# Performance work log

Measured on AMD Instinct MI355X. Metric: run time of the kernel, lower is better.

## Reference

```python
import jax, jax.numpy as jnp
import numpy as np

C_CT, C_MRI, C_OUT = 64, 64, 64
B, D, H, W = 1, 8, 32, 32


def setup_inputs() -> dict:
    key = jax.random.key(0)
    ks = jax.random.split(key, 18)
    s = 0.05
    inp = {
        "ct_features": jax.random.normal(ks[0], (B, C_CT, D, H, W), jnp.float32),
        "mri_features": jax.random.normal(ks[1], (B, C_MRI, D, H, W), jnp.float32),
        # 1x1x1 Conv3d == per-voxel linear: weight (out, in), bias (out,)
        "wq_ct": jax.random.normal(ks[2], (C_OUT, C_CT), jnp.float32) * s,
        "bq_ct": jax.random.normal(ks[3], (C_OUT,), jnp.float32) * s,
        "wk_mri": jax.random.normal(ks[4], (C_OUT, C_MRI), jnp.float32) * s,
        "bk_mri": jax.random.normal(ks[5], (C_OUT,), jnp.float32) * s,
        "wv_mri": jax.random.normal(ks[6], (C_OUT, C_MRI), jnp.float32) * s,
        "bv_mri": jax.random.normal(ks[7], (C_OUT,), jnp.float32) * s,
        "wq_mri": jax.random.normal(ks[8], (C_OUT, C_MRI), jnp.float32) * s,
        "bq_mri": jax.random.normal(ks[9], (C_OUT,), jnp.float32) * s,
        "wk_ct": jax.random.normal(ks[10], (C_OUT, C_CT), jnp.float32) * s,
        "bk_ct": jax.random.normal(ks[11], (C_OUT,), jnp.float32) * s,
        "wv_ct": jax.random.normal(ks[12], (C_OUT, C_CT), jnp.float32) * s,
        "bv_ct": jax.random.normal(ks[13], (C_OUT,), jnp.float32) * s,
        "wo": jax.random.normal(ks[14], (C_OUT, 2 * C_OUT), jnp.float32) * s,
        "bo": jax.random.normal(ks[15], (C_OUT,), jnp.float32) * s,
    }
    return inp


def _proj(x_flat, w, b):
    # x_flat: (B, Cin, N); 1x1x1 conv -> (B, Cout, N)
    return jnp.einsum("oc,bcn->bon", w, x_flat) + b[None, :, None]


def _forward(ct, mri, wq_ct, bq_ct, wk_mri, bk_mri, wv_mri, bv_mri,
             wq_mri, bq_mri, wk_ct, bk_ct, wv_ct, bv_ct, wo, bo):
    b, _, d, h, w = ct.shape
    n = d * h * w
    ct_f = ct.reshape(b, ct.shape[1], n)
    mri_f = mri.reshape(b, mri.shape[1], n)
    scale = 1.0 / np.sqrt(C_OUT).astype(np.float32)

    # CT queries attend over MRI keys/values
    ct_q = _proj(ct_f, wq_ct, bq_ct)      # (B, C, N)
    mri_k = _proj(mri_f, wk_mri, bk_mri)  # (B, C, N)
    mri_v = _proj(mri_f, wv_mri, bv_mri)  # (B, C, N)
    attn_ct = jax.nn.softmax(jnp.einsum("bci,bcj->bij", ct_q, mri_k) * scale, axis=-1)
    ct_att = jnp.einsum("bcj,bij->bci", mri_v, attn_ct)  # (B, C, N)

    # MRI queries attend over CT keys/values
    mri_q = _proj(mri_f, wq_mri, bq_mri)
    ct_k = _proj(ct_f, wk_ct, bk_ct)
    ct_v = _proj(ct_f, wv_ct, bv_ct)
    attn_mri = jax.nn.softmax(jnp.einsum("bci,bcj->bij", mri_q, ct_k) * scale, axis=-1)
    mri_att = jnp.einsum("bcj,bij->bci", ct_v, attn_mri)

    fused = jnp.concatenate([ct_att, mri_att], axis=1)  # (B, 2C, N)
    out = _proj(fused, wo, bo)  # (B, C, N)
    return out.reshape(b, C_OUT, d, h, w)


def reference(ct_features, mri_features, wq_ct, bq_ct, wk_mri, bk_mri,
              wv_mri, bv_mri, wq_mri, bq_mri, wk_ct, bk_ct, wv_ct, bv_ct,
              wo, bo):
    return _forward(ct_features, mri_features, wq_ct, bq_ct, wk_mri, bk_mri,
                    wv_mri, bv_mri, wq_mri, bq_mri, wk_ct, bk_ct,
                    wv_ct, bv_ct, wo, bo)
```

## Files before the change

### kernel.cpp

```cpp
#include <hip/hip_runtime.h>
#include <stdint.h>

constexpr int N = 8192;
constexpr float QSCALE = 0.18033688011112042f;
constexpr int SPLIT = 4;

typedef __attribute__((ext_vector_type(4))) float f32x4;
typedef __attribute__((ext_vector_type(4))) unsigned int u32x4;
typedef __attribute__((ext_vector_type(2))) unsigned int u32x2;
typedef __attribute__((ext_vector_type(4))) unsigned short u16x4;

__device__ inline unsigned short f2bf(float f) {
  unsigned u = __builtin_bit_cast(unsigned, f);
  u += 0x7FFFu + ((u >> 16) & 1u);
  return (unsigned short)(u >> 16);
}
__device__ inline float bf2f(unsigned short u) {
  return __builtin_bit_cast(float, (unsigned)u << 16);
}
__device__ inline unsigned cvtpk(float a, float b) {
  unsigned r;
  asm("v_cvt_pk_bf16_f32 %0, %1, %2" : "=v"(r) : "v"(a), "v"(b));
  return r;
}

__device__ inline void mfma16x16x32bf16(f32x4& d, u32x4 a, u32x4 b) {
  asm volatile("v_mfma_f32_16x16x32_bf16 %0, %1, %2, %0" : "+v"(d) : "v"(a), "v"(b));
}
__device__ inline void mfma_guard() {
  __builtin_amdgcn_sched_barrier(0);
  asm volatile("s_nop 7\n\ts_nop 7");
  __builtin_amdgcn_sched_barrier(0);
}
__device__ inline void gload16(const void* src, void* lds) {
  __builtin_amdgcn_global_load_lds(
      (const __attribute__((address_space(1))) unsigned int*)src,
      (__attribute__((address_space(3))) unsigned int*)lds, 16, 0, 0);
}

struct ProjArgs {
  const float* x[6];
  const float* w[6];
  const float* b[6];
  unsigned short* o[6];
  int mode[6];
  float scale[6];
};

__global__ __launch_bounds__(256) void proj_kernel(ProjArgs A) {
  const int p = blockIdx.y;
  const float* __restrict__ x = A.x[p];
  const float* __restrict__ w = A.w[p];
  const float* __restrict__ bias = A.b[p];
  unsigned short* __restrict__ out = A.o[p];
  const int n0 = blockIdx.x * 64;
  __shared__ float Xs[64][64];
  __shared__ float Ws[64][64];
  const int t = threadIdx.x;
#pragma unroll
  for (int i = 0; i < 4; i++) {
    int s = t + i * 256;
    ((u32x4*)Ws)[s] = ((const u32x4*)w)[s];
  }
#pragma unroll
  for (int i = 0; i < 4; i++) {
    int s = t + i * 256;
    int c = s >> 4, nc = s & 15;
    *(u32x4*)&Xs[c][nc * 4] = *(const u32x4*)&x[c * N + n0 + nc * 4];
  }
  __syncthreads();
  const int n = t & 63, h = t >> 6;
  float acc[16];
#pragma unroll
  for (int o = 0; o < 16; o++) acc[o] = bias[h * 16 + o];
  for (int c = 0; c < 64; c++) {
    float xv = Xs[c][n];
#pragma unroll
    for (int o = 0; o < 16; o++) acc[o] = fmaf(Ws[h * 16 + o][c], xv, acc[o]);
  }
  const float sc = A.scale[p];
  if (A.mode[p] == 0) {
    unsigned short* po = out + (size_t)(n0 + n) * 64 + h * 16;
#pragma unroll
    for (int o = 0; o < 16; o++) po[o] = f2bf(acc[o] * sc);
  } else {
#pragma unroll
    for (int o = 0; o < 16; o++) out[(size_t)(h * 16 + o) * N + n0 + n] = f2bf(acc[o] * sc);
  }
}

__global__ __launch_bounds__(256, 2) void attn_kernel(
    const unsigned short* __restrict__ Q0, const unsigned short* __restrict__ K0,
    const unsigned short* __restrict__ V0, const unsigned short* __restrict__ Q1,
    const unsigned short* __restrict__ K1, const unsigned short* __restrict__ V1,
    unsigned short* __restrict__ Opart, float* __restrict__ Lsum) {
  const int bid = blockIdx.x;
  const int slice = bid & 7;
  const int qb = bid >> 3;
  const int dir = slice >> 2;
  const int chunk = slice & 3;
  const unsigned short* __restrict__ Q = dir ? Q1 : Q0;
  const unsigned short* __restrict__ K = dir ? K1 : K0;
  const unsigned short* __restrict__ V = dir ? V1 : V0;

  __shared__ char smem[65536];

  const int t = threadIdx.x;
  const int lane = t & 63, w = t >> 6;
  const int g = lane >> 4, sl = lane & 15;
  char* const pw = smem + 49152 + w * 4096;
  const int kvbase = chunk * 2048;

  const int srowoff = (lane >> 3);
  const int swzb = ((lane & 7) ^ (lane >> 3)) * 16;
  const char* const Kc = (const char*)K;
  const char* const Vc = (const char*)V;

  u32x4 qf[2][2];
#pragma unroll
  for (int rb = 0; rb < 2; rb++) {
    const int qrow = qb * 128 + w * 32 + rb * 16 + sl;
#pragma unroll
    for (int ks = 0; ks < 2; ks++)
      qf[rb][ks] = *(const u32x4*)(Q + (size_t)qrow * 64 + ks * 32 + 8 * g);
  }

  f32x4 acc[4][2];
#pragma unroll
  for (int mb = 0; mb < 4; mb++)
#pragma unroll
    for (int rb = 0; rb < 2; rb++)
#pragma unroll
      for (int r = 0; r < 4; r++) acc[mb][rb][r] = 0.f;
  float lpart[2] = {0.f, 0.f};

#pragma unroll
  for (int tt = 0; tt < 2; tt++) {
    const int j0 = kvbase + tt * 64;
#pragma unroll
    for (int i = 0; i < 2; i++) {
      const int row = (w * 2 + i) * 8 + srowoff;
      gload16(Kc + (size_t)(j0 + row) * 128 + swzb,
              smem + tt * 8192 + (w * 2 + i) * 1024);
      gload16(Vc + (size_t)row * (N * 2) + (size_t)j0 * 2 + swzb,
              smem + 24576 + tt * 8192 + (w * 2 + i) * 1024);
    }
  }

  int cur = 0;
  for (int jt = 0; jt < 32; ++jt) {
    if (jt < 31) asm volatile("s_waitcnt vmcnt(4)" ::: "memory");
    else         asm volatile("s_waitcnt vmcnt(0)" ::: "memory");
    __builtin_amdgcn_s_barrier();
    __builtin_amdgcn_sched_barrier(0);

    if (jt + 2 < 32) {
      const int j0n = kvbase + (jt + 2) * 64;
      const int nb = (cur >= 1) ? cur - 1 : 2;
#pragma unroll
      for (int i = 0; i < 2; i++) {
        const int row = (w * 2 + i) * 8 + srowoff;
        gload16(Kc + (size_t)(j0n + row) * 128 + swzb,
                smem + nb * 8192 + (w * 2 + i) * 1024);
        gload16(Vc + (size_t)row * (N * 2) + (size_t)j0n * 2 + swzb,
                smem + 24576 + nb * 8192 + (w * 2 + i) * 1024);
      }
    }
    char* const Kl = smem + cur * 8192;
    char* const Vl = smem + 24576 + cur * 8192;

    u32x4 kf[4][2];
#pragma unroll
    for (int jb = 0; jb < 4; jb++) {
      const int row = jb * 16 + sl;
      const int rs = (row & 7) << 4;
#pragma unroll
      for (int ks = 0; ks < 2; ks++)
        kf[jb][ks] = *(const u32x4*)(Kl + row * 128 + ((ks * 64 + 16 * g) ^ rs));
    }

    f32x4 st[4][2];
    __builtin_amdgcn_s_setprio(1);
#pragma unroll
    for (int jb = 0; jb < 4; jb++)
#pragma unroll
      for (int rb = 0; rb < 2; rb++) {
#pragma unroll
        for (int r = 0; r < 4; r++) st[jb][rb][r] = 0.f;
        mfma16x16x32bf16(st[jb][rb], kf[jb][0], qf[rb][0]);
        mfma16x16x32bf16(st[jb][rb], kf[jb][1], qf[rb][1]);
      }
    __builtin_amdgcn_s_setprio(0);
    mfma_guard();

    u32x4 vf[4][2];
#pragma unroll
    for (int mb = 0; mb < 4; mb++) {
      const int row = mb * 16 + sl;
      const int rs = (row & 7) << 4;
#pragma unroll
      for (int ks = 0; ks < 2; ks++)
        vf[mb][ks] = *(const u32x4*)(Vl + row * 128 + ((ks * 64 + 16 * g) ^ rs));
    }

#pragma unroll
    for (int rb = 0; rb < 2; rb++) {
      const int q = rb * 16 + sl;
      const int qswz = (q & 7) << 4;
#pragma unroll
      for (int jb = 0; jb < 4; jb++) {
        float e0 = __builtin_amdgcn_exp2f(st[jb][rb][0]);
        float e1 = __builtin_amdgcn_exp2f(st[jb][rb][1]);
        float e2 = __builtin_amdgcn_exp2f(st[jb][rb][2]);
        float e3 = __builtin_amdgcn_exp2f(st[jb][rb][3]);
        lpart[rb] += (e0 + e1) + (e2 + e3);
        u32x2 pk;
        pk[0] = cvtpk(e0, e1);
        pk[1] = cvtpk(e2, e3);
        *(u32x2*)(pw + q * 128 + ((jb * 32 + 8 * g) ^ qswz)) = pk;
      }
    }

    u32x4 pf[2][2];
#pragma unroll
    for (int rb = 0; rb < 2; rb++) {
      const int q = rb * 16 + sl;
      const int qswz = (q & 7) << 4;
      pf[rb][0] = *(const u32x4*)(pw + q * 128 + ((16 * g) ^ qswz));
      pf[rb][1] = *(const u32x4*)(pw + q * 128 + ((64 + 16 * g) ^ qswz));
    }
    __builtin_amdgcn_s_setprio(1);
#pragma unroll
    for (int mb = 0; mb < 4; mb++)
#pragma unroll
      for (int rb = 0; rb < 2; rb++) {
        mfma16x16x32bf16(acc[mb][rb], vf[mb][0], pf[rb][0]);
        mfma16x16x32bf16(acc[mb][rb], vf[mb][1], pf[rb][1]);
      }
    __builtin_amdgcn_s_setprio(0);

    cur = (cur < 2) ? cur + 1 : 0;
  }
  mfma_guard();

#pragma unroll
  for (int rb = 0; rb < 2; rb++) {
    lpart[rb] += __shfl_xor(lpart[rb], 16);
    lpart[rb] += __shfl_xor(lpart[rb], 32);
  }

#pragma unroll
  for (int rb = 0; rb < 2; rb++) {
    const int q = rb * 16 + sl;
    const int qg = qb * 128 + w * 32 + q;
    const size_t pbase = ((size_t)slice * N + qg) * 64;
#pragma unroll
    for (int mb = 0; mb < 4; mb++) {
      u32x2 pk;
      pk[0] = cvtpk(acc[mb][rb][0], acc[mb][rb][1]);
      pk[1] = cvtpk(acc[mb][rb][2], acc[mb][rb][3]);
      *(u32x2*)(Opart + pbase + mb * 16 + 4 * g) = pk;
    }
    if (g == 0) Lsum[(size_t)slice * N + qg] = lpart[rb];
  }
}

__global__ __launch_bounds__(256) void oproj_kernel(
    const unsigned short* __restrict__ Opart, const float* __restrict__ Lsum,
    const float* __restrict__ wo, const float* __restrict__ bo,
    float* __restrict__ out) {
  __shared__ float Fs[128][32];
  __shared__ float Ws[64][128];
  const int t = threadIdx.x;
  const int n0 = blockIdx.x * 32;
#pragma unroll
  for (int i = 0; i < 8; i++) {
    int s = t + i * 256;
    ((u32x4*)Ws)[s] = ((const u32x4*)wo)[s];
  }
  const int q = t & 31;
  const int cg = t >> 5;
#pragma unroll
  for (int dir = 0; dir < 2; dir++) {
    float lt = 0.f;
#pragma unroll
    for (int c = 0; c < 4; c++) lt += Lsum[(size_t)(dir * SPLIT + c) * N + n0 + q];
    const float rD = 1.0f / lt;
#pragma unroll
    for (int i = 0; i < 2; i++) {
      const int ch4 = cg * 2 + i;
      float s0 = 0.f, s1 = 0.f, s2 = 0.f, s3 = 0.f;
#pragma unroll
      for (int c = 0; c < 4; c++) {
        u16x4 v = *(const u16x4*)(Opart +
            ((size_t)(dir * SPLIT + c) * N + n0 + q) * 64 + ch4 * 4);
        s0 += bf2f(v[0]); s1 += bf2f(v[1]); s2 += bf2f(v[2]); s3 += bf2f(v[3]);
      }
      Fs[dir * 64 + ch4 * 4 + 0][q] = s0 * rD;
      Fs[dir * 64 + ch4 * 4 + 1][q] = s1 * rD;
      Fs[dir * 64 + ch4 * 4 + 2][q] = s2 * rD;
      Fs[dir * 64 + ch4 * 4 + 3][q] = s3 * rD;
    }
  }
  __syncthreads();
  const int n = t & 31, h = t >> 5;
  float acc[8];
#pragma unroll
  for (int o = 0; o < 8; o++) acc[o] = bo[h * 8 + o];
  for (int ch = 0; ch < 128; ch++) {
    float fv = Fs[ch][n];
#pragma unroll
    for (int o = 0; o < 8; o++) acc[o] = fmaf(Ws[h * 8 + o][ch], fv, acc[o]);
  }
#pragma unroll
  for (int o = 0; o < 8; o++) out[(size_t)(h * 8 + o) * N + n0 + n] = acc[o];
}

extern "C" void kernel_launch(void* const* d_in, const int* in_sizes, int n_in,
                              void* d_out, int out_size, void* d_ws, size_t ws_size,
                              hipStream_t stream) {
  const float* ct     = (const float*)d_in[0];
  const float* mri    = (const float*)d_in[1];
  const float* wq_ct  = (const float*)d_in[2];
  const float* bq_ct  = (const float*)d_in[3];
  const float* wk_mri = (const float*)d_in[4];
  const float* bk_mri = (const float*)d_in[5];
  const float* wv_mri = (const float*)d_in[6];
  const float* bv_mri = (const float*)d_in[7];
  const float* wq_mri = (const float*)d_in[8];
  const float* bq_mri = (const float*)d_in[9];
  const float* wk_ct  = (const float*)d_in[10];
  const float* bk_ct  = (const float*)d_in[11];
  const float* wv_ct  = (const float*)d_in[12];
  const float* bv_ct  = (const float*)d_in[13];
  const float* wo     = (const float*)d_in[14];
  const float* bo     = (const float*)d_in[15];

  char* ws = (char*)d_ws;
  const size_t MB = (size_t)1 << 20;
  unsigned short* Qt_ct  = (unsigned short*)(ws + 0 * MB);
  unsigned short* Kt_mri = (unsigned short*)(ws + 1 * MB);
  unsigned short* V_mri  = (unsigned short*)(ws + 2 * MB);
  unsigned short* Qt_mri = (unsigned short*)(ws + 3 * MB);
  unsigned short* Kt_ct  = (unsigned short*)(ws + 4 * MB);
  unsigned short* V_ct   = (unsigned short*)(ws + 5 * MB);
  unsigned short* Opart  = (unsigned short*)(ws + 6 * MB);
  float* Lsum            = (float*)(ws + 14 * MB);

  ProjArgs A;
  A.x[0] = ct;  A.w[0] = wq_ct;  A.b[0] = bq_ct;  A.o[0] = Qt_ct;  A.mode[0] = 0; A.scale[0] = QSCALE;
  A.x[1] = mri; A.w[1] = wk_mri; A.b[1] = bk_mri; A.o[1] = Kt_mri; A.mode[1] = 0; A.scale[1] = 1.f;
  A.x[2] = mri; A.w[2] = wv_mri; A.b[2] = bv_mri; A.o[2] = V_mri;  A.mode[2] = 1; A.scale[2] = 1.f;
  A.x[3] = mri; A.w[3] = wq_mri; A.b[3] = bq_mri; A.o[3] = Qt_mri; A.mode[3] = 0; A.scale[3] = QSCALE;
  A.x[4] = ct;  A.w[4] = wk_ct;  A.b[4] = bk_ct;  A.o[4] = Kt_ct;  A.mode[4] = 0; A.scale[4] = 1.f;
  A.x[5] = ct;  A.w[5] = wv_ct;  A.b[5] = bv_ct;  A.o[5] = V_ct;   A.mode[5] = 1; A.scale[5] = 1.f;

  proj_kernel<<<dim3(128, 6), 256, 0, stream>>>(A);
  attn_kernel<<<dim3(512), 256, 0, stream>>>(Qt_ct, Kt_mri, V_mri,
                                             Qt_mri, Kt_ct, V_ct, Opart, Lsum);
  oproj_kernel<<<dim3(256), 256, 0, stream>>>(Opart, Lsum, wo, bo, (float*)d_out);
}
```

Baseline: 73.80 us.

## Split KV tile across wave pairs in attention kernel, halve queries per block

Each block now handles 64 queries instead of 128, with pairs of waves sharing a query slab and each taking half of every 64-key tile. The two halves' partial outputs and row sums are combined through shared memory at the end. The K/V pipeline drops from triple to double buffering, which cuts LDS to about 38KB and lets launch bounds ask for 4 blocks per CU on a grid twice as large. The aim is more occupancy and parallelism, paid for with an extra LDS reduction, barriers and a shallower prefetch.

```diff
diff --git a/kernel.cpp b/kernel.cpp
--- a/kernel.cpp
+++ b/kernel.cpp
@@ -89,7 +89,7 @@
   }
 }
 
-__global__ __launch_bounds__(256, 2) void attn_kernel(
+__global__ __launch_bounds__(256, 4) void attn_kernel(
     const unsigned short* __restrict__ Q0, const unsigned short* __restrict__ K0,
     const unsigned short* __restrict__ V0, const unsigned short* __restrict__ Q1,
     const unsigned short* __restrict__ K1, const unsigned short* __restrict__ V1,
@@ -103,15 +103,16 @@
   const unsigned short* __restrict__ K = dir ? K1 : K0;
   const unsigned short* __restrict__ V = dir ? V1 : V0;
 
-  __shared__ char smem[65536];
+  __shared__ char smem[38912];
 
   const int t = threadIdx.x;
   const int lane = t & 63, w = t >> 6;
+  const int qsub = w >> 1, cw = w & 1;
   const int g = lane >> 4, sl = lane & 15;
-  char* const pw = smem + 49152 + w * 4096;
+  char* const pw = smem + 32768 + w * 1280;
   const int kvbase = chunk * 2048;
 
-  const int srowoff = (lane >> 3);
+  const int srowoff = lane >> 3;
   const int swzb = ((lane & 7) ^ (lane >> 3)) * 16;
   const char* const Kc = (const char*)K;
   const char* const Vc = (const char*)V;
@@ -119,7 +120,7 @@
   u32x4 qf[2][2];
 #pragma unroll
   for (int rb = 0; rb < 2; rb++) {
-    const int qrow = qb * 128 + w * 32 + rb * 16 + sl;
+    const int qrow = qb * 64 + qsub * 32 + rb * 16 + sl;
 #pragma unroll
     for (int ks = 0; ks < 2; ks++)
       qf[rb][ks] = *(const u32x4*)(Q + (size_t)qrow * 64 + ks * 32 + 8 * g);
@@ -135,54 +136,49 @@
   float lpart[2] = {0.f, 0.f};
 
 #pragma unroll
-  for (int tt = 0; tt < 2; tt++) {
-    const int j0 = kvbase + tt * 64;
-#pragma unroll
-    for (int i = 0; i < 2; i++) {
-      const int row = (w * 2 + i) * 8 + srowoff;
-      gload16(Kc + (size_t)(j0 + row) * 128 + swzb,
-              smem + tt * 8192 + (w * 2 + i) * 1024);
-      gload16(Vc + (size_t)row * (N * 2) + (size_t)j0 * 2 + swzb,
-              smem + 24576 + tt * 8192 + (w * 2 + i) * 1024);
-    }
-  }
-
-  int cur = 0;
+  for (int i = 0; i < 2; i++) {
+    const int row = (w * 2 + i) * 8 + srowoff;
+    gload16(Kc + (size_t)(kvbase + row) * 128 + swzb,
+            smem + (w * 2 + i) * 1024);
+    gload16(Vc + (size_t)row * (N * 2) + (size_t)kvbase * 2 + swzb,
+            smem + 16384 + (w * 2 + i) * 1024);
+  }
+
   for (int jt = 0; jt < 32; ++jt) {
-    if (jt < 31) asm volatile("s_waitcnt vmcnt(4)" ::: "memory");
-    else         asm volatile("s_waitcnt vmcnt(0)" ::: "memory");
+    asm volatile("s_waitcnt vmcnt(0)" ::: "memory");
     __builtin_amdgcn_s_barrier();
     __builtin_amdgcn_sched_barrier(0);
-
-    if (jt + 2 < 32) {
-      const int j0n = kvbase + (jt + 2) * 64;
-      const int nb = (cur >= 1) ? cur - 1 : 2;
+    const int cur = jt & 1;
+
+    if (jt + 1 < 32) {
+      const int j0n = kvbase + (jt + 1) * 64;
+      const int nb = cur ^ 1;
 #pragma unroll
       for (int i = 0; i < 2; i++) {
         const int row = (w * 2 + i) * 8 + srowoff;
         gload16(Kc + (size_t)(j0n + row) * 128 + swzb,
                 smem + nb * 8192 + (w * 2 + i) * 1024);
         gload16(Vc + (size_t)row * (N * 2) + (size_t)j0n * 2 + swzb,
-                smem + 24576 + nb * 8192 + (w * 2 + i) * 1024);
+                smem + 16384 + nb * 8192 + (w * 2 + i) * 1024);
       }
     }
     char* const Kl = smem + cur * 8192;
-    char* const Vl = smem + 24576 + cur * 8192;
-
-    u32x4 kf[4][2];
-#pragma unroll
-    for (int jb = 0; jb < 4; jb++) {
-      const int row = jb * 16 + sl;
+    char* const Vl = smem + 16384 + cur * 8192;
+
+    u32x4 kf[2][2];
+#pragma unroll
+    for (int jb = 0; jb < 2; jb++) {
+      const int row = cw * 32 + jb * 16 + sl;
       const int rs = (row & 7) << 4;
 #pragma unroll
       for (int ks = 0; ks < 2; ks++)
         kf[jb][ks] = *(const u32x4*)(Kl + row * 128 + ((ks * 64 + 16 * g) ^ rs));
     }
 
-    f32x4 st[4][2];
+    f32x4 st[2][2];
     __builtin_amdgcn_s_setprio(1);
 #pragma unroll
-    for (int jb = 0; jb < 4; jb++)
+    for (int jb = 0; jb < 2; jb++)
 #pragma unroll
       for (int rb = 0; rb < 2; rb++) {
 #pragma unroll
@@ -193,22 +189,18 @@
     __builtin_amdgcn_s_setprio(0);
     mfma_guard();
 
-    u32x4 vf[4][2];
+    u32x4 vf[4];
 #pragma unroll
     for (int mb = 0; mb < 4; mb++) {
       const int row = mb * 16 + sl;
       const int rs = (row & 7) << 4;
-#pragma unroll
-      for (int ks = 0; ks < 2; ks++)
-        vf[mb][ks] = *(const u32x4*)(Vl + row * 128 + ((ks * 64 + 16 * g) ^ rs));
+      vf[mb] = *(const u32x4*)(Vl + row * 128 + ((cw * 64 + 16 * g) ^ rs));
     }
 
 #pragma unroll
     for (int rb = 0; rb < 2; rb++) {
-      const int q = rb * 16 + sl;
-      const int qswz = (q & 7) << 4;
-#pragma unroll
-      for (int jb = 0; jb < 4; jb++) {
+#pragma unroll
+      for (int jb = 0; jb < 2; jb++) {
         float e0 = __builtin_amdgcn_exp2f(st[jb][rb][0]);
         float e1 = __builtin_amdgcn_exp2f(st[jb][rb][1]);
         float e2 = __builtin_amdgcn_exp2f(st[jb][rb][2]);
@@ -217,51 +209,57 @@
         u32x2 pk;
         pk[0] = cvtpk(e0, e1);
         pk[1] = cvtpk(e2, e3);
-        *(u32x2*)(pw + q * 128 + ((jb * 32 + 8 * g) ^ qswz)) = pk;
-      }
-    }
-
-    u32x4 pf[2][2];
+        *(u32x2*)(pw + sl * 80 + jb * 32 + 8 * g) = pk;
+      }
+      u32x4 pf = *(const u32x4*)(pw + sl * 80 + 16 * g);
+      __builtin_amdgcn_s_setprio(1);
+#pragma unroll
+      for (int mb = 0; mb < 4; mb++)
+        mfma16x16x32bf16(acc[mb][rb], vf[mb], pf);
+      __builtin_amdgcn_s_setprio(0);
+    }
+  }
+  mfma_guard();
+
+#pragma unroll
+  for (int rb = 0; rb < 2; rb++) {
+    lpart[rb] += __shfl_xor(lpart[rb], 16);
+    lpart[rb] += __shfl_xor(lpart[rb], 32);
+  }
+
+  __syncthreads();
+  char* const obuf = smem + qsub * 8192;
+  float* const mlb = (float*)(smem + 32768);
+  if (cw == 1) {
 #pragma unroll
     for (int rb = 0; rb < 2; rb++) {
       const int q = rb * 16 + sl;
       const int qswz = (q & 7) << 4;
-      pf[rb][0] = *(const u32x4*)(pw + q * 128 + ((16 * g) ^ qswz));
-      pf[rb][1] = *(const u32x4*)(pw + q * 128 + ((64 + 16 * g) ^ qswz));
-    }
-    __builtin_amdgcn_s_setprio(1);
-#pragma unroll
-    for (int mb = 0; mb < 4; mb++)
-#pragma unroll
-      for (int rb = 0; rb < 2; rb++) {
-        mfma16x16x32bf16(acc[mb][rb], vf[mb][0], pf[rb][0]);
-        mfma16x16x32bf16(acc[mb][rb], vf[mb][1], pf[rb][1]);
-      }
-    __builtin_amdgcn_s_setprio(0);
-
-    cur = (cur < 2) ? cur + 1 : 0;
-  }
-  mfma_guard();
-
-#pragma unroll
-  for (int rb = 0; rb < 2; rb++) {
-    lpart[rb] += __shfl_xor(lpart[rb], 16);
-    lpart[rb] += __shfl_xor(lpart[rb], 32);
-  }
-
-#pragma unroll
-  for (int rb = 0; rb < 2; rb++) {
-    const int q = rb * 16 + sl;
-    const int qg = qb * 128 + w * 32 + q;
-    const size_t pbase = ((size_t)slice * N + qg) * 64;
-#pragma unroll
-    for (int mb = 0; mb < 4; mb++) {
-      u32x2 pk;
-      pk[0] = cvtpk(acc[mb][rb][0], acc[mb][rb][1]);
-      pk[1] = cvtpk(acc[mb][rb][2], acc[mb][rb][3]);
-      *(u32x2*)(Opart + pbase + mb * 16 + 4 * g) = pk;
-    }
-    if (g == 0) Lsum[(size_t)slice * N + qg] = lpart[rb];
+#pragma unroll
+      for (int mb = 0; mb < 4; mb++)
+        *(f32x4*)(obuf + q * 256 + (((mb * 16 + 4 * g) * 4) ^ qswz)) = acc[mb][rb];
+      if (g == 0) mlb[qsub * 32 + q] = lpart[rb];
+    }
+  }
+  __syncthreads();
+  if (cw == 0) {
+#pragma unroll
+    for (int rb = 0; rb < 2; rb++) {
+      const int q = rb * 16 + sl;
+      const int qswz = (q & 7) << 4;
+      const float ltot = lpart[rb] + mlb[qsub * 32 + q];
+      const int qg = qb * 64 + qsub * 32 + q;
+      const size_t pbase = ((size_t)slice * N + qg) * 64;
+#pragma unroll
+      for (int mb = 0; mb < 4; mb++) {
+        f32x4 oo = *(const f32x4*)(obuf + q * 256 + (((mb * 16 + 4 * g) * 4) ^ qswz));
+        u32x2 pk;
+        pk[0] = cvtpk(acc[mb][rb][0] + oo[0], acc[mb][rb][1] + oo[1]);
+        pk[1] = cvtpk(acc[mb][rb][2] + oo[2], acc[mb][rb][3] + oo[3]);
+        *(u32x2*)(Opart + pbase + mb * 16 + 4 * g) = pk;
+      }
+      if (g == 0) Lsum[(size_t)slice * N + qg] = ltot;
+    }
   }
 }
 
@@ -356,7 +354,7 @@
   A.x[5] = ct;  A.w[5] = wv_ct;  A.b[5] = bv_ct;  A.o[5] = V_ct;   A.mode[5] = 1; A.scale[5] = 1.f;
 
   proj_kernel<<<dim3(128, 6), 256, 0, stream>>>(A);
-  attn_kernel<<<dim3(512), 256, 0, stream>>>(Qt_ct, Kt_mri, V_mri,
-                                             Qt_mri, Kt_ct, V_ct, Opart, Lsum);
+  attn_kernel<<<dim3(1024), 256, 0, stream>>>(Qt_ct, Kt_mri, V_mri,
+                                              Qt_mri, Kt_ct, V_ct, Opart, Lsum);
   oproj_kernel<<<dim3(256), 256, 0, stream>>>(Opart, Lsum, wo, bo, (float*)d_out);
 }
```

Result: slower. 75.56 us (+2.4%).

## Use 128-key tiles with double buffering and padded per-row P staging

Applied to the files above, without the earlier changes.

The attention main loop now processes 128-key tiles (16 iterations) instead of 64-key tiles (32 iterations), with a double-buffered smem stage instead of triple-buffered. The P scratch is reduced to one 16-row strip per wave with a padded 144-byte row stride in place of an XOR swizzle. The V tile is stored 256 bytes per row with a new swizzle. The aim is fewer barriers and waits per key and interleaved exp/PV work per half-tile. In exchange it waits on vmcnt(0) each iteration, which leaves less prefetch depth. LDS use rises to about 73 KB, which may hurt the occupancy of 2 blocks per CU.

```diff
diff --git a/kernel.cpp b/kernel.cpp
--- a/kernel.cpp
+++ b/kernel.cpp
@@ -103,19 +103,35 @@
   const unsigned short* __restrict__ K = dir ? K1 : K0;
   const unsigned short* __restrict__ V = dir ? V1 : V0;
 
-  __shared__ char smem[65536];
+  __shared__ char smem[74752];
 
   const int t = threadIdx.x;
   const int lane = t & 63, w = t >> 6;
   const int g = lane >> 4, sl = lane & 15;
-  char* const pw = smem + 49152 + w * 4096;
+  char* const pw = smem + 65536 + w * 2304;
   const int kvbase = chunk * 2048;
 
-  const int srowoff = (lane >> 3);
-  const int swzb = ((lane & 7) ^ (lane >> 3)) * 16;
+  const int srowoff = lane >> 3;
+  const int kswz = ((lane & 7) ^ (lane >> 3)) * 16;
+  const int vchsub = lane >> 4;
+  const int vc16 = lane & 15;
   const char* const Kc = (const char*)K;
   const char* const Vc = (const char*)V;
 
+#define STAGE(jtile, slot)                                                     \
+  do {                                                                         \
+    const int j0s = kvbase + (jtile) * 128;                                    \
+    _Pragma("unroll") for (int i = 0; i < 4; i++) {                            \
+      const int krow = (w * 4 + i) * 8 + srowoff;                              \
+      gload16(Kc + (size_t)(j0s + krow) * 128 + kswz,                          \
+              smem + (slot) * 16384 + (w * 4 + i) * 1024);                     \
+      const int vch = (w * 4 + i) * 4 + vchsub;                                \
+      gload16(Vc + (size_t)vch * (N * 2) + (size_t)j0s * 2 +                   \
+                  ((vc16 ^ (vch & 7)) * 16),                                   \
+              smem + 32768 + (slot) * 16384 + (w * 4 + i) * 1024);             \
+    }                                                                          \
+  } while (0)
+
   u32x4 qf[2][2];
 #pragma unroll
   for (int rb = 0; rb < 2; rb++) {
@@ -134,113 +150,80 @@
       for (int r = 0; r < 4; r++) acc[mb][rb][r] = 0.f;
   float lpart[2] = {0.f, 0.f};
 
-#pragma unroll
-  for (int tt = 0; tt < 2; tt++) {
-    const int j0 = kvbase + tt * 64;
-#pragma unroll
-    for (int i = 0; i < 2; i++) {
-      const int row = (w * 2 + i) * 8 + srowoff;
-      gload16(Kc + (size_t)(j0 + row) * 128 + swzb,
-              smem + tt * 8192 + (w * 2 + i) * 1024);
-      gload16(Vc + (size_t)row * (N * 2) + (size_t)j0 * 2 + swzb,
-              smem + 24576 + tt * 8192 + (w * 2 + i) * 1024);
-    }
-  }
-
-  int cur = 0;
-  for (int jt = 0; jt < 32; ++jt) {
-    if (jt < 31) asm volatile("s_waitcnt vmcnt(4)" ::: "memory");
-    else         asm volatile("s_waitcnt vmcnt(0)" ::: "memory");
+  STAGE(0, 0);
+  for (int jt = 0; jt < 16; ++jt) {
+    asm volatile("s_waitcnt vmcnt(0)" ::: "memory");
     __builtin_amdgcn_s_barrier();
     __builtin_amdgcn_sched_barrier(0);
-
-    if (jt + 2 < 32) {
-      const int j0n = kvbase + (jt + 2) * 64;
-      const int nb = (cur >= 1) ? cur - 1 : 2;
-#pragma unroll
-      for (int i = 0; i < 2; i++) {
-        const int row = (w * 2 + i) * 8 + srowoff;
-        gload16(Kc + (size_t)(j0n + row) * 128 + swzb,
-                smem + nb * 8192 + (w * 2 + i) * 1024);
-        gload16(Vc + (size_t)row * (N * 2) + (size_t)j0n * 2 + swzb,
-                smem + 24576 + nb * 8192 + (w * 2 + i) * 1024);
+    const int cur = jt & 1;
+    if (jt + 1 < 16) STAGE(jt + 1, cur ^ 1);
+    char* const Kl = smem + cur * 16384;
+    char* const Vl = smem + 32768 + cur * 16384;
+
+    f32x4 st[2][4][2];
+#pragma unroll
+    for (int h = 0; h < 2; h++) {
+      u32x4 kf[4][2];
+#pragma unroll
+      for (int jb = 0; jb < 4; jb++) {
+        const int row = h * 64 + jb * 16 + sl;
+        const int rs = (row & 7) << 4;
+#pragma unroll
+        for (int ks = 0; ks < 2; ks++)
+          kf[jb][ks] = *(const u32x4*)(Kl + row * 128 + ((ks * 64 + 16 * g) ^ rs));
+      }
+      __builtin_amdgcn_s_setprio(1);
+#pragma unroll
+      for (int jb = 0; jb < 4; jb++)
+#pragma unroll
+        for (int rb = 0; rb < 2; rb++) {
+#pragma unroll
+          for (int r = 0; r < 4; r++) st[h][jb][rb][r] = 0.f;
+          mfma16x16x32bf16(st[h][jb][rb], kf[jb][0], qf[rb][0]);
+          mfma16x16x32bf16(st[h][jb][rb], kf[jb][1], qf[rb][1]);
+        }
+      __builtin_amdgcn_s_setprio(0);
+    }
+
+#pragma unroll
+    for (int h = 0; h < 2; h++) {
+      u32x4 vf[4][2];
+#pragma unroll
+      for (int mb = 0; mb < 4; mb++) {
+        const int row = mb * 16 + sl;
+        const int rs = (row & 7) << 4;
+#pragma unroll
+        for (int ks = 0; ks < 2; ks++)
+          vf[mb][ks] = *(const u32x4*)(Vl + row * 256 +
+                                       ((h * 128 + ks * 64 + 16 * g) ^ rs));
+      }
+#pragma unroll
+      for (int rb = 0; rb < 2; rb++) {
+#pragma unroll
+        for (int jb = 0; jb < 4; jb++) {
+          float e0 = __builtin_amdgcn_exp2f(st[h][jb][rb][0]);
+          float e1 = __builtin_amdgcn_exp2f(st[h][jb][rb][1]);
+          float e2 = __builtin_amdgcn_exp2f(st[h][jb][rb][2]);
+          float e3 = __builtin_amdgcn_exp2f(st[h][jb][rb][3]);
+          lpart[rb] += (e0 + e1) + (e2 + e3);
+          u32x2 pk;
+          pk[0] = cvtpk(e0, e1);
+          pk[1] = cvtpk(e2, e3);
+          *(u32x2*)(pw + sl * 144 + jb * 32 + 8 * g) = pk;
+        }
+        u32x4 pf0 = *(const u32x4*)(pw + sl * 144 + 16 * g);
+        u32x4 pf1 = *(const u32x4*)(pw + sl * 144 + 64 + 16 * g);
+        __builtin_amdgcn_s_setprio(1);
+#pragma unroll
+        for (int mb = 0; mb < 4; mb++) {
+          mfma16x16x32bf16(acc[mb][rb], vf[mb][0], pf0);
+          mfma16x16x32bf16(acc[mb][rb], vf[mb][1], pf1);
+        }
+        __builtin_amdgcn_s_setprio(0);
       }
     }
-    char* const Kl = smem + cur * 8192;
-    char* const Vl = smem + 24576 + cur * 8192;
-
-    u32x4 kf[4][2];
-#pragma unroll
-    for (int jb = 0; jb < 4; jb++) {
-      const int row = jb * 16 + sl;
-      const int rs = (row & 7) << 4;
-#pragma unroll
-      for (int ks = 0; ks < 2; ks++)
-        kf[jb][ks] = *(const u32x4*)(Kl + row * 128 + ((ks * 64 + 16 * g) ^ rs));
-    }
-
-    f32x4 st[4][2];
-    __builtin_amdgcn_s_setprio(1);
-#pragma unroll
-    for (int jb = 0; jb < 4; jb++)
-#pragma unroll
-      for (int rb = 0; rb < 2; rb++) {
-#pragma unroll
-        for (int r = 0; r < 4; r++) st[jb][rb][r] = 0.f;
-        mfma16x16x32bf16(st[jb][rb], kf[jb][0], qf[rb][0]);
-        mfma16x16x32bf16(st[jb][rb], kf[jb][1], qf[rb][1]);
-      }
-    __builtin_amdgcn_s_setprio(0);
-    mfma_guard();
-
-    u32x4 vf[4][2];
-#pragma unroll
-    for (int mb = 0; mb < 4; mb++) {
-      const int row = mb * 16 + sl;
-      const int rs = (row & 7) << 4;
-#pragma unroll
-      for (int ks = 0; ks < 2; ks++)
-        vf[mb][ks] = *(const u32x4*)(Vl + row * 128 + ((ks * 64 + 16 * g) ^ rs));
-    }
-
-#pragma unroll
-    for (int rb = 0; rb < 2; rb++) {
-      const int q = rb * 16 + sl;
-      const int qswz = (q & 7) << 4;
-#pragma unroll
-      for (int jb = 0; jb < 4; jb++) {
-        float e0 = __builtin_amdgcn_exp2f(st[jb][rb][0]);
-        float e1 = __builtin_amdgcn_exp2f(st[jb][rb][1]);
-        float e2 = __builtin_amdgcn_exp2f(st[jb][rb][2]);
-        float e3 = __builtin_amdgcn_exp2f(st[jb][rb][3]);
-        lpart[rb] += (e0 + e1) + (e2 + e3);
-        u32x2 pk;
-        pk[0] = cvtpk(e0, e1);
-        pk[1] = cvtpk(e2, e3);
-        *(u32x2*)(pw + q * 128 + ((jb * 32 + 8 * g) ^ qswz)) = pk;
-      }
-    }
-
-    u32x4 pf[2][2];
-#pragma unroll
-    for (int rb = 0; rb < 2; rb++) {
-      const int q = rb * 16 + sl;
-      const int qswz = (q & 7) << 4;
-      pf[rb][0] = *(const u32x4*)(pw + q * 128 + ((16 * g) ^ qswz));
-      pf[rb][1] = *(const u32x4*)(pw + q * 128 + ((64 + 16 * g) ^ qswz));
-    }
-    __builtin_amdgcn_s_setprio(1);
-#pragma unroll
-    for (int mb = 0; mb < 4; mb++)
-#pragma unroll
-      for (int rb = 0; rb < 2; rb++) {
-        mfma16x16x32bf16(acc[mb][rb], vf[mb][0], pf[rb][0]);
-        mfma16x16x32bf16(acc[mb][rb], vf[mb][1], pf[rb][1]);
-      }
-    __builtin_amdgcn_s_setprio(0);
-
-    cur = (cur < 2) ? cur + 1 : 0;
-  }
+  }
+#undef STAGE
   mfma_guard();
 
 #pragma unroll
```

After: 72.66 us. About the same (-1.5%).
